# Kernel optimization log

Hardware: AMD Instinct MI355X
Metric: run time of the kernel (lower is better)

Reference implementation:

```python
import jax, jax.numpy as jnp
import numpy as np
import math

B, T, D = 8, 1024, 1024
N, L = 256, 768
H = 16
TE = 2048  # time_embed_dim
EPS = 1e-5


def _ln(x, g, b):
    mu = jnp.mean(x, axis=-1, keepdims=True)
    var = jnp.mean(jnp.square(x - mu), axis=-1, keepdims=True)
    return (x - mu) * jax.lax.rsqrt(var + EPS) * g + b


def setup_inputs() -> dict:
    key = jax.random.key(0)
    ks = jax.random.split(key, 16)
    s = lambda fan_in: 1.0 / math.sqrt(fan_in)
    return {
        "x": jax.random.normal(ks[0], (B, T, D), jnp.float32),
        "xf": jax.random.normal(ks[1], (B, N, L), jnp.float32),
        "emb": jax.random.normal(ks[2], (B, TE), jnp.float32),
        "ln_g": jnp.ones((D,), jnp.float32),
        "ln_b": jnp.zeros((D,), jnp.float32),
        "cln_g": jnp.ones((L,), jnp.float32),
        "cln_b": jnp.zeros((L,), jnp.float32),
        "Wq": jax.random.normal(ks[3], (D, D), jnp.float32) * s(D),
        "bq": jnp.zeros((D,), jnp.float32),
        "Wk": jax.random.normal(ks[4], (L, D), jnp.float32) * s(L),
        "bk": jnp.zeros((D,), jnp.float32),
        "Wv": jax.random.normal(ks[5], (L, D), jnp.float32) * s(L),
        "bv": jnp.zeros((D,), jnp.float32),
        "sln_g": jnp.ones((D,), jnp.float32),
        "sln_b": jnp.zeros((D,), jnp.float32),
        "Wemb": jax.random.normal(ks[6], (TE, 2 * D), jnp.float32) * s(TE),
        "bemb": jnp.zeros((2 * D,), jnp.float32),
        "Wout": jax.random.normal(ks[7], (D, D), jnp.float32) * s(D) * 0.02,
        "bout": jnp.zeros((D,), jnp.float32),
    }


def reference(x, xf, emb, ln_g, ln_b, cln_g, cln_b, Wq, bq, Wk, bk, Wv, bv,
              sln_g, sln_b, Wemb, bemb, Wout, bout):
    # x: (B,T,D), xf: (B,N,L), emb: (B,TE)
    hd = D // H
    q = (_ln(x, ln_g, ln_b) @ Wq + bq).reshape(B, T, H, hd)
    xf_n = _ln(xf, cln_g, cln_b)
    k = (xf_n @ Wk + bk).reshape(B, N, H, hd)
    v = (xf_n @ Wv + bv).reshape(B, N, H, hd)
    # scores: (B,T,N,H); note: scaled by sqrt(D//H)
    att = jnp.einsum('bthd,bnhd->btnh', q, k) / math.sqrt(hd)
    w = jax.nn.softmax(att, axis=2)  # softmax over conditioning tokens N
    y = jnp.einsum('btnh,bnhd->bthd', w, v).reshape(B, T, D)
    # StylizationBlock (dropout = 0)
    emb_out = jax.nn.silu(emb) @ Wemb + bemb  # (B, 2D)
    scale, shift = jnp.split(emb_out[:, None, :], 2, axis=2)
    h = _ln(y, sln_g, sln_b) * (1.0 + scale) + shift
    h = jax.nn.silu(h) @ Wout + bout
    return x + h
```

## Files before the change

### kernel.cpp

```cpp
#include <hip/hip_runtime.h>
#include <hip/hip_bf16.h>

typedef __hip_bfloat16 bf16;
typedef unsigned short ushort;
typedef unsigned char uchar;
typedef long i64;
typedef __attribute__((ext_vector_type(4))) float f32x4;

#define B_ 8
#define T_ 1024
#define D_ 1024
#define N_ 256
#define L_ 768
#define H_ 16
#define HD_ 64
#define TE_ 2048

__device__ __forceinline__ void gld16(const void* g, void* l) {
    __builtin_amdgcn_global_load_lds((const __attribute__((address_space(1))) void*)g,
                                     (__attribute__((address_space(3))) void*)l,
                                     16, 0, 0);
}

__device__ __forceinline__ float bitf(unsigned u) { return __uint_as_float(u); }

__device__ __forceinline__ int pk4_fp8(float a, float b, float c, float d) {
    int p = __builtin_amdgcn_cvt_pk_fp8_f32(a, b, 0, false);
    p = __builtin_amdgcn_cvt_pk_fp8_f32(c, d, p, true);
    return p;
}
__device__ __forceinline__ uchar pk1_fp8(float a) {
    int p = __builtin_amdgcn_cvt_pk_fp8_f32(a, a, 0, false);
    return (uchar)(p & 0xff);
}
__device__ __forceinline__ float dec8(uchar b) {
    int e = (b >> 3) & 15, m = b & 7;
    float mag = e ? (float)(8 + m) * bitf((unsigned)(117 + e) << 23)
                  : (float)m * bitf(118u << 23);
    return (b & 0x80) ? -mag : mag;
}

template <int NV>
__device__ __forceinline__ void ln_row(const float* __restrict__ rp,
                                       const float* __restrict__ g,
                                       const float* __restrict__ bb,
                                       uchar* __restrict__ op, int lane) {
    float4 va[NV];
#pragma unroll
    for (int i = 0; i < NV; i++) va[i] = ((const float4*)rp)[i * 64 + lane];
    float s = 0.f, s2 = 0.f;
#pragma unroll
    for (int i = 0; i < NV; i++) {
        s  += va[i].x + va[i].y + va[i].z + va[i].w;
        s2 += va[i].x * va[i].x + va[i].y * va[i].y + va[i].z * va[i].z + va[i].w * va[i].w;
    }
#pragma unroll
    for (int off = 32; off; off >>= 1) {
        s  += __shfl_xor(s,  off, 64);
        s2 += __shfl_xor(s2, off, 64);
    }
    const float inv_n = 1.f / (float)(NV * 256);
    float mu = s * inv_n;
    float var = s2 * inv_n - mu * mu;
    float rstd = rsqrtf(var + 1e-5f);
#pragma unroll
    for (int i = 0; i < NV; i++) {
        float4 gv = ((const float4*)g)[i * 64 + lane];
        float4 bv = ((const float4*)bb)[i * 64 + lane];
        ((int*)op)[i * 64 + lane] = pk4_fp8((va[i].x - mu) * rstd * gv.x + bv.x,
                                            (va[i].y - mu) * rstd * gv.y + bv.y,
                                            (va[i].z - mu) * rstd * gv.z + bv.z,
                                            (va[i].w - mu) * rstd * gv.w + bv.w);
    }
}

__global__ __launch_bounds__(256) void prep_kernel(
        const float* __restrict__ x, const float* __restrict__ xf,
        const float* __restrict__ g1, const float* __restrict__ b1,
        const float* __restrict__ g2, const float* __restrict__ b2,
        const float* __restrict__ Wq, const float* __restrict__ Wk,
        const float* __restrict__ Wv, const float* __restrict__ Wo,
        const float* __restrict__ emb, const float* __restrict__ Wemb,
        uchar* __restrict__ xn8, uchar* __restrict__ xfn8,
        uchar* __restrict__ wq8, uchar* __restrict__ wk8,
        uchar* __restrict__ wv8, uchar* __restrict__ wo8,
        float* __restrict__ part) {
    __shared__ __align__(16) char smem[16384];
    int bid = blockIdx.x;
    int tid = threadIdx.x;
    if (bid < 2560) {
        int w = tid >> 6, lane = tid & 63;
        int row = bid * 4 + w;
        if (row < B_ * T_) {
            ln_row<4>(x + (size_t)row * D_, g1, b1, xn8 + (size_t)row * D_, lane);
        } else {
            int r = row - B_ * T_;
            ln_row<3>(xf + (size_t)r * L_, g2, b2, xfn8 + (size_t)r * L_, lane);
        }
    } else if (bid < 3456) {
        uchar (*t)[65] = (uchar(*)[65])smem;
        int id = bid - 2560;
        int xb = id & 15, y = id >> 4;
        const float* W; uchar* Wt; int K, ky;
        if (y < 16)      { W = Wq; Wt = wq8; K = 1024; ky = y; }
        else if (y < 28) { W = Wk; Wt = wk8; K = 768;  ky = y - 16; }
        else if (y < 40) { W = Wv; Wt = wv8; K = 768;  ky = y - 28; }
        else             { W = Wo; Wt = wo8; K = 1024; ky = y - 40; }
        int k0 = ky * 64, n0 = xb * 64;
#pragma unroll
        for (int i = 0; i < 16; i++) {
            int e = tid + i * 256;
            int r = e >> 6, c = e & 63;
            t[r][c] = pk1_fp8(W[(size_t)(k0 + r) * D_ + n0 + c]);
        }
        __syncthreads();
#pragma unroll
        for (int i = 0; i < 4; i++) {
            int e = tid + i * 256;
            int r = e >> 4, cg = (e & 15) * 4;
            unsigned u = (unsigned)t[cg][r] | ((unsigned)t[cg + 1][r] << 8)
                       | ((unsigned)t[cg + 2][r] << 16) | ((unsigned)t[cg + 3][r] << 24);
            *(unsigned*)&Wt[(size_t)(n0 + r) * K + k0 + cg] = u;
        }
    } else {
        float* se  = (float*)smem;
        float* red = (float*)(smem + 8192);
        int id = bid - 3456;
        int j0 = (id & 31) * 64;
        int ks = id >> 5;
        int tx = tid & 15, ty = tid >> 4;
        int w = tid >> 6, lane = tid & 63;
#pragma unroll
        for (int b = 0; b < 8; b++) {
            float xv = emb[b * TE_ + ks * 256 + tid];
            se[b * 256 + tid] = xv / (1.f + __expf(-xv));
        }
        __syncthreads();
        float acc[8][4] = {};
#pragma unroll 4
        for (int i = 0; i < 16; i++) {
            int e = ty + 16 * i;
            float4 wv = *(const float4*)&Wemb[(size_t)(ks * 256 + e) * 2048 + j0 + tx * 4];
#pragma unroll
            for (int b = 0; b < 8; b++) {
                float s = se[b * 256 + e];
                acc[b][0] += s * wv.x; acc[b][1] += s * wv.y;
                acc[b][2] += s * wv.z; acc[b][3] += s * wv.w;
            }
        }
#pragma unroll
        for (int b = 0; b < 8; b++)
#pragma unroll
            for (int m = 0; m < 4; m++) {
                float v = acc[b][m];
                v += __shfl_down(v, 32, 64);
                v += __shfl_down(v, 16, 64);
                if (lane < 16) red[(w * 8 + b) * 64 + lane * 4 + m] = v;
            }
        __syncthreads();
        for (int o = tid; o < 512; o += 256) {
            int b = o >> 6, jl = o & 63;
            float s = red[(0 * 8 + b) * 64 + jl] + red[(1 * 8 + b) * 64 + jl]
                    + red[(2 * 8 + b) * 64 + jl] + red[(3 * 8 + b) * 64 + jl];
            part[((size_t)ks * 8 + b) * 2048 + j0 + jl] = s;
        }
    }
}

template <int MODE>
__device__ __forceinline__ void gemm_body(const uchar* __restrict__ Ap,
                                          const uchar* __restrict__ Bp,
                                          const float* __restrict__ bias,
                                          const float* __restrict__ res,
                                          void* __restrict__ Cout,
                                          int m0, int n0, int Ncols, int K,
                                          uchar* SH) {
    int tid = threadIdx.x;
    int w = tid >> 6, lane = tid & 63;
    int quad = lane >> 4, l15 = lane & 15;
    int wm = (w >> 1) * 64, wn = (w & 1) * 64;
    int lr4 = lane >> 2;
    int sp4 = lane & 3;
    uchar* A0 = SH;
    uchar* B0 = SH + 8192;
    uchar* A1 = SH + 16384;
    uchar* B1 = SH + 24576;
    f32x4 acc[4][4] = {};

    auto stage = [&](int kt, uchar* As, uchar* Bs) {
#pragma unroll
        for (int j = 0; j < 2; j++) {
            int r = w * 32 + j * 16 + lr4;
            int gc = sp4 ^ (r & 3);
            gld16(&Ap[(size_t)(m0 + r) * K + kt + gc * 16], &As[(w * 32 + j * 16) * 64]);
        }
#pragma unroll
        for (int j = 0; j < 2; j++) {
            int r = w * 32 + j * 16 + lr4;
            int gc = sp4 ^ (r & 3);
            gld16(&Bp[(size_t)(n0 + r) * K + kt + gc * 16], &Bs[(w * 32 + j * 16) * 64]);
        }
    };
    auto compute = [&](const uchar* As, const uchar* Bs) {
#pragma unroll
        for (int kh = 0; kh < 2; kh++) {
            int c4 = kh * 2 + (quad >> 1);
            int sub = (quad & 1) * 8;
            int pos = (c4 ^ (l15 & 3)) * 16 + sub;
            i64 af[4], bfr[4];
#pragma unroll
            for (int mt = 0; mt < 4; mt++)
                af[mt] = *(const i64*)&As[(wm + mt * 16 + l15) * 64 + pos];
#pragma unroll
            for (int nt = 0; nt < 4; nt++)
                bfr[nt] = *(const i64*)&Bs[(wn + nt * 16 + l15) * 64 + pos];
#pragma unroll
            for (int mt = 0; mt < 4; mt++)
#pragma unroll
                for (int nt = 0; nt < 4; nt++)
                    acc[mt][nt] = __builtin_amdgcn_mfma_f32_16x16x32_fp8_fp8(af[mt], bfr[nt], acc[mt][nt], 0, 0, 0);
        }
    };

    int nt2 = K >> 6;
    stage(0, A0, B0);
    __syncthreads();
    for (int t = 0; t + 2 <= nt2; t += 2) {
        stage((t + 1) * 64, A1, B1);
        compute(A0, B0);
        __syncthreads();
        if (t + 2 < nt2) stage((t + 2) * 64, A0, B0);
        compute(A1, B1);
        __syncthreads();
    }

    if (MODE == 0) {
#pragma unroll
        for (int mt = 0; mt < 4; mt++)
#pragma unroll
            for (int nt = 0; nt < 4; nt++)
#pragma unroll
                for (int reg = 0; reg < 4; reg++) {
                    int rl = wm + mt * 16 + quad * 4 + reg;
                    int cl = wn + nt * 16 + l15;
                    SH[rl * 128 + cl] = pk1_fp8(acc[mt][nt][reg] + bias[n0 + cl]);
                }
        __syncthreads();
#pragma unroll
        for (int i = 0; i < 4; i++) {
            int row = (tid >> 3) + i * 32;
            int ch = (tid & 7) * 16;
            *(int4*)&((uchar*)Cout)[(size_t)(m0 + row) * Ncols + n0 + ch] =
                *(const int4*)&SH[row * 128 + ch];
        }
    } else {
#pragma unroll
        for (int mt = 0; mt < 4; mt++) {
#pragma unroll
            for (int nt = 0; nt < 4; nt++) {
#pragma unroll
                for (int reg = 0; reg < 4; reg++) {
                    int row = m0 + wm + mt * 16 + quad * 4 + reg;
                    int col = n0 + wn + nt * 16 + l15;
                    float v = acc[mt][nt][reg] + bias[col];
                    if (MODE == 1) {
                        v += res[(size_t)row * Ncols + col];
                        ((float*)Cout)[(size_t)row * Ncols + col] = v;
                    } else {
                        int b = row >> 8, n = row & 255;
                        int h = col >> 6, d = col & 63;
                        size_t addr = ((size_t)(b * 16 + h)) * 16384 + (size_t)d * 256
                                    + (((n >> 4) ^ (d & 15)) * 16) + (n & 15);
                        ((uchar*)Cout)[addr] = pk1_fp8(v);
                    }
                }
            }
        }
    }
}

__global__ __launch_bounds__(256, 4) void qkv_gemm(const uchar* __restrict__ xn8,
                                                   const uchar* __restrict__ xfn8,
                                                   const uchar* __restrict__ wq8,
                                                   const uchar* __restrict__ wk8,
                                                   const uchar* __restrict__ wv8,
                                                   const float* __restrict__ bq,
                                                   const float* __restrict__ bk,
                                                   const float* __restrict__ bv,
                                                   uchar* __restrict__ q8,
                                                   uchar* __restrict__ k8,
                                                   uchar* __restrict__ vT8,
                                                   const float* __restrict__ part,
                                                   const float* __restrict__ bemb,
                                                   float* __restrict__ embo) {
    __shared__ __align__(16) uchar SH[32768];
    int bid = blockIdx.x;
    if (bid < 512) {
        gemm_body<0>(xn8, wq8, bq, nullptr, q8,
                     (bid & 63) * 128, (bid >> 6) * 128, D_, D_, SH);
    } else if (bid < 640) {
        int id = bid - 512;
        gemm_body<0>(xfn8, wk8, bk, nullptr, k8,
                     (id & 15) * 128, (id >> 4) * 128, D_, L_, SH);
    } else if (bid < 768) {
        int id = bid - 640;
        gemm_body<2>(xfn8, wv8, bv, nullptr, vT8,
                     (id & 15) * 128, (id >> 4) * 128, D_, L_, SH);
    } else {
        int o = (bid - 768) * 256 + threadIdx.x;
        int b = o >> 11, j = o & 2047;
        float s = bemb[j];
#pragma unroll
        for (int ks = 0; ks < 8; ks++) s += part[((size_t)ks * 8 + b) * 2048 + j];
        embo[o] = s;
    }
}

__global__ __launch_bounds__(256, 4) void out_gemm(const uchar* __restrict__ a8,
                                                   const uchar* __restrict__ wo8,
                                                   const float* __restrict__ bout,
                                                   const float* __restrict__ x,
                                                   float* __restrict__ out) {
    __shared__ __align__(16) uchar SH[32768];
    int bid = blockIdx.x;
    gemm_body<1>(a8, wo8, bout, x, out,
                 (bid & 63) * 128, (bid >> 6) * 128, D_, D_, SH);
}

__global__ __launch_bounds__(256) void attn_mfma(const uchar* __restrict__ q8,
                                                 const uchar* __restrict__ k8,
                                                 const uchar* __restrict__ vT8,
                                                 uchar* __restrict__ y8) {
    __shared__ __align__(16) uchar KV[16384];
    __shared__ __align__(16) uchar P[16384];
    int tid = threadIdx.x;
    int w = tid >> 6, lane = tid & 63;
    int quad = lane >> 4, l15 = lane & 15;
    int bid = blockIdx.x;
    int work = (bid & 7) * 256 + (bid >> 3);
    int t0 = (work & 15) * 64;
    int bh = work >> 4;
    int b = bh >> 4, h = bh & 15;
    int lln = lane >> 3, sp = lane & 7;

#pragma unroll
    for (int j = 0; j < 4; j++) {
        int dn = w * 32 + j * 8 + lln;
        int c8 = sp ^ (dn & 7);
        int n = dn * 2 + (c8 >> 2);
        gld16(&k8[(size_t)(b * N_ + n) * D_ + h * 64 + (c8 & 3) * 16],
              &KV[(w * 32 + j * 8) * 128]);
    }
#pragma unroll
    for (int j = 0; j < 2; j++) {
        int r = w * 16 + j * 8 + lln;
        int c = (sp ^ (r & 7)) & 3;
        gld16(&q8[(size_t)(b * T_ + t0 + r) * D_ + h * 64 + c * 16],
              &P[(w * 16 + j * 8) * 128]);
    }
    __syncthreads();

    int qrow = w * 16 + l15;
    i64 aq[2];
#pragma unroll
    for (int kk2 = 0; kk2 < 2; kk2++) {
        int chunk = kk2 * 2 + (quad >> 1);
        aq[kk2] = *(const i64*)&P[qrow * 128 + ((chunk ^ (qrow & 7)) * 16) + (quad & 1) * 8];
    }
    f32x4 sf[16];
#pragma unroll
    for (int nt = 0; nt < 16; nt++) {
        int n = nt * 16 + l15;
        int dn = n >> 1, hn = n & 1;
        int c80 = (hn * 4 + 0 + (quad >> 1)) ^ (dn & 7);
        int c81 = (hn * 4 + 2 + (quad >> 1)) ^ (dn & 7);
        i64 b0 = *(const i64*)&KV[dn * 128 + c80 * 16 + (quad & 1) * 8];
        i64 b1 = *(const i64*)&KV[dn * 128 + c81 * 16 + (quad & 1) * 8];
        f32x4 z = {};
        f32x4 t = __builtin_amdgcn_mfma_f32_16x16x32_fp8_fp8(aq[0], b0, z, 0, 0, 0);
        sf[nt] = __builtin_amdgcn_mfma_f32_16x16x32_fp8_fp8(aq[1], b1, t, 0, 0, 0);
    }
    __syncthreads();

    const uchar* vbase = vT8 + (size_t)(b * 16 + h) * 16384;
#pragma unroll
    for (int j = 0; j < 4; j++) {
        gld16(&vbase[(w * 4 + j) * 1024 + lane * 16], &KV[(w * 4 + j) * 1024]);
    }

    const float scale = 0.125f;
    float sm[4] = {0.f, 0.f, 0.f, 0.f};
#pragma unroll
    for (int nt = 0; nt < 16; nt++)
#pragma unroll
        for (int reg = 0; reg < 4; reg++) {
            float e = __expf(sf[nt][reg] * scale);
            sf[nt][reg] = e;
            sm[reg] += e;
        }
#pragma unroll
    for (int off = 1; off < 16; off <<= 1)
#pragma unroll
        for (int reg = 0; reg < 4; reg++)
            sm[reg] += __shfl_xor(sm[reg], off, 64);
    float inv[4];
#pragma unroll
    for (int reg = 0; reg < 4; reg++) inv[reg] = 1.f / sm[reg];

#pragma unroll
    for (int nt = 0; nt < 16; nt++)
#pragma unroll
        for (int reg = 0; reg < 4; reg++) {
            int r = w * 16 + quad * 4 + reg;
            int n = nt * 16 + l15;
            P[r * 256 + (((n >> 4) ^ (r & 15)) * 16) + (n & 15)] = pk1_fp8(sf[nt][reg]);
        }
    __syncthreads();

    f32x4 of[4] = {};
    int prow = w * 16 + l15;
#pragma unroll
    for (int kk = 0; kk < 8; kk++) {
        int ck = kk * 2 + (quad >> 1);
        i64 ap = *(const i64*)&P[prow * 256 + ((ck ^ (prow & 15)) * 16) + (quad & 1) * 8];
#pragma unroll
        for (int dt = 0; dt < 4; dt++) {
            int d = dt * 16 + l15;
            i64 bv = *(const i64*)&KV[d * 256 + ((ck ^ (d & 15)) * 16) + (quad & 1) * 8];
            of[dt] = __builtin_amdgcn_mfma_f32_16x16x32_fp8_fp8(ap, bv, of[dt], 0, 0, 0);
        }
    }
    __syncthreads();
#pragma unroll
    for (int dt = 0; dt < 4; dt++)
#pragma unroll
        for (int reg = 0; reg < 4; reg++) {
            int rl = w * 16 + quad * 4 + reg;
            P[rl * 64 + dt * 16 + l15] = pk1_fp8(of[dt][reg] * inv[reg]);
        }
    __syncthreads();
    {
        int row = tid >> 2, ch = (tid & 3) * 16;
        *(int4*)&y8[(size_t)(b * T_ + t0 + row) * D_ + h * 64 + ch] =
            *(const int4*)&P[row * 64 + ch];
    }
}

__global__ __launch_bounds__(256) void styl_kernel(const uchar* __restrict__ y8,
                                                   const float* __restrict__ g,
                                                   const float* __restrict__ bb,
                                                   const float* __restrict__ embo,
                                                   uchar* __restrict__ a8) {
    int tid = threadIdx.x, w = tid >> 6, lane = tid & 63;
    int row = blockIdx.x * 4 + w;
    int b = row >> 10;
    const uchar* rp = y8 + (size_t)row * D_;
    uchar* op = a8 + (size_t)row * D_;
    float v[16];
    float s = 0.f, s2 = 0.f;
#pragma unroll
    for (int i = 0; i < 4; i++) {
        unsigned u = ((const unsigned*)rp)[i * 64 + lane];
#pragma unroll
        for (int j = 0; j < 4; j++) {
            float f = dec8((uchar)(u >> (8 * j)));
            v[i * 4 + j] = f; s += f; s2 += f * f;
        }
    }
#pragma unroll
    for (int off = 32; off; off >>= 1) {
        s  += __shfl_xor(s,  off, 64);
        s2 += __shfl_xor(s2, off, 64);
    }
    float mu = s * (1.f / 1024.f);
    float rstd = rsqrtf(s2 * (1.f / 1024.f) - mu * mu + 1e-5f);
#pragma unroll
    for (int i = 0; i < 4; i++) {
        int c4 = i * 64 + lane;
        float4 gv  = ((const float4*)g)[c4];
        float4 bv  = ((const float4*)bb)[c4];
        float4 scv = ((const float4*)(embo + b * 2048))[c4];
        float4 shv = ((const float4*)(embo + b * 2048 + 1024))[c4];
        float h0 = (v[i*4+0] - mu) * rstd * gv.x + bv.x;
        float h1 = (v[i*4+1] - mu) * rstd * gv.y + bv.y;
        float h2 = (v[i*4+2] - mu) * rstd * gv.z + bv.z;
        float h3 = (v[i*4+3] - mu) * rstd * gv.w + bv.w;
        h0 = h0 * (1.f + scv.x) + shv.x;
        h1 = h1 * (1.f + scv.y) + shv.y;
        h2 = h2 * (1.f + scv.z) + shv.z;
        h3 = h3 * (1.f + scv.w) + shv.w;
        h0 = h0 / (1.f + __expf(-h0));
        h1 = h1 / (1.f + __expf(-h1));
        h2 = h2 / (1.f + __expf(-h2));
        h3 = h3 / (1.f + __expf(-h3));
        ((int*)op)[c4] = pk4_fp8(h0, h1, h2, h3);
    }
}

extern "C" void kernel_launch(void* const* d_in, const int* in_sizes, int n_in,
                              void* d_out, int out_size, void* d_ws, size_t ws_size,
                              hipStream_t stream) {
    const float* x    = (const float*)d_in[0];
    const float* xf   = (const float*)d_in[1];
    const float* emb  = (const float*)d_in[2];
    const float* ln_g = (const float*)d_in[3];
    const float* ln_b = (const float*)d_in[4];
    const float* cln_g= (const float*)d_in[5];
    const float* cln_b= (const float*)d_in[6];
    const float* Wq   = (const float*)d_in[7];
    const float* bq   = (const float*)d_in[8];
    const float* Wk   = (const float*)d_in[9];
    const float* bk   = (const float*)d_in[10];
    const float* Wv   = (const float*)d_in[11];
    const float* bv   = (const float*)d_in[12];
    const float* sln_g= (const float*)d_in[13];
    const float* sln_b= (const float*)d_in[14];
    const float* Wemb = (const float*)d_in[15];
    const float* bemb = (const float*)d_in[16];
    const float* Wout = (const float*)d_in[17];
    const float* bout = (const float*)d_in[18];
    float* out = (float*)d_out;

    char* wsp = (char*)d_ws;
    const size_t MB = 1024 * 1024;
    uchar* xn8  = (uchar*)(wsp);
    uchar* xfn8 = (uchar*)(wsp + 8 * MB);
    uchar* wq8  = (uchar*)(wsp + 10 * MB);
    uchar* wk8  = (uchar*)(wsp + 11 * MB);
    uchar* wv8  = (uchar*)(wsp + 12 * MB);
    uchar* wo8  = (uchar*)(wsp + 13 * MB);
    uchar* q8   = (uchar*)(wsp + 14 * MB);
    uchar* k8   = (uchar*)(wsp + 22 * MB);
    uchar* vT8  = (uchar*)(wsp + 24 * MB);
    uchar* y8   = (uchar*)(wsp + 26 * MB);
    uchar* a8   = (uchar*)(wsp + 34 * MB);
    float* embo = (float*)(wsp + 42 * MB);
    float* part = (float*)(wsp + 43 * MB);

    prep_kernel<<<3712, 256, 0, stream>>>(x, xf, ln_g, ln_b, cln_g, cln_b,
                                          Wq, Wk, Wv, Wout, emb, Wemb,
                                          xn8, xfn8, wq8, wk8, wv8, wo8, part);

    qkv_gemm<<<832, 256, 0, stream>>>(xn8, xfn8, wq8, wk8, wv8, bq, bk, bv,
                                      q8, k8, vT8, part, bemb, embo);

    attn_mfma<<<2048, 256, 0, stream>>>(q8, k8, vT8, y8);

    styl_kernel<<<2048, 256, 0, stream>>>(y8, sln_g, sln_b, embo, a8);

    out_gemm<<<512, 256, 0, stream>>>(a8, wo8, bout, x, out);
}
```

Before: 233.8 us.

## Transpose attention MFMA operands to keep softmax probabilities in registers

Swaps the A/B operands of the QK^T MFMA so each lane holds a query's scores across keys, which turns the row-sum into two cross-lane shuffles. The exponentiated probabilities are packed to fp8 and redistributed with lane shuffles straight into MFMA operand registers for the PV product, removing the LDS round trip for P and one barrier. The output tile is written to LDS with an XOR swizzle, and the P buffer shrinks to 8 KB, lowering LDS use. The cost is extra shuffle and select instructions inside the PV loop.

```diff
diff --git a/kernel.cpp b/kernel.cpp
--- a/kernel.cpp
+++ b/kernel.cpp
@@ -332,7 +332,7 @@
                                                  const uchar* __restrict__ vT8,
                                                  uchar* __restrict__ y8) {
     __shared__ __align__(16) uchar KV[16384];
-    __shared__ __align__(16) uchar P[16384];
+    __shared__ __align__(16) uchar P[8192];
     int tid = threadIdx.x;
     int w = tid >> 6, lane = tid & 63;
     int quad = lane >> 4, l15 = lane & 15;
@@ -361,12 +361,14 @@
     __syncthreads();
 
     int qrow = w * 16 + l15;
-    i64 aq[2];
-#pragma unroll
-    for (int kk2 = 0; kk2 < 2; kk2++) {
-        int chunk = kk2 * 2 + (quad >> 1);
-        aq[kk2] = *(const i64*)&P[qrow * 128 + ((chunk ^ (qrow & 7)) * 16) + (quad & 1) * 8];
-    }
+    i64 aq0, aq1;
+    {
+        int c0 = (quad >> 1);
+        int c1 = 2 + (quad >> 1);
+        aq0 = *(const i64*)&P[qrow * 128 + ((c0 ^ (qrow & 7)) * 16) + (quad & 1) * 8];
+        aq1 = *(const i64*)&P[qrow * 128 + ((c1 ^ (qrow & 7)) * 16) + (quad & 1) * 8];
+    }
+
     f32x4 sf[16];
 #pragma unroll
     for (int nt = 0; nt < 16; nt++) {
@@ -377,8 +379,8 @@
         i64 b0 = *(const i64*)&KV[dn * 128 + c80 * 16 + (quad & 1) * 8];
         i64 b1 = *(const i64*)&KV[dn * 128 + c81 * 16 + (quad & 1) * 8];
         f32x4 z = {};
-        f32x4 t = __builtin_amdgcn_mfma_f32_16x16x32_fp8_fp8(aq[0], b0, z, 0, 0, 0);
-        sf[nt] = __builtin_amdgcn_mfma_f32_16x16x32_fp8_fp8(aq[1], b1, t, 0, 0, 0);
+        f32x4 t = __builtin_amdgcn_mfma_f32_16x16x32_fp8_fp8(b0, aq0, z, 0, 0, 0);
+        sf[nt] = __builtin_amdgcn_mfma_f32_16x16x32_fp8_fp8(b1, aq1, t, 0, 0, 0);
     }
     __syncthreads();
 
@@ -389,60 +391,52 @@
     }
 
     const float scale = 0.125f;
-    float sm[4] = {0.f, 0.f, 0.f, 0.f};
+    float sm = 0.f;
 #pragma unroll
     for (int nt = 0; nt < 16; nt++)
 #pragma unroll
         for (int reg = 0; reg < 4; reg++) {
             float e = __expf(sf[nt][reg] * scale);
             sf[nt][reg] = e;
-            sm[reg] += e;
-        }
-#pragma unroll
-    for (int off = 1; off < 16; off <<= 1)
-#pragma unroll
-        for (int reg = 0; reg < 4; reg++)
-            sm[reg] += __shfl_xor(sm[reg], off, 64);
-    float inv[4];
-#pragma unroll
-    for (int reg = 0; reg < 4; reg++) inv[reg] = 1.f / sm[reg];
-
-#pragma unroll
-    for (int nt = 0; nt < 16; nt++)
-#pragma unroll
-        for (int reg = 0; reg < 4; reg++) {
-            int r = w * 16 + quad * 4 + reg;
-            int n = nt * 16 + l15;
-            P[r * 256 + (((n >> 4) ^ (r & 15)) * 16) + (n & 15)] = pk1_fp8(sf[nt][reg]);
-        }
+            sm += e;
+        }
+    sm += __shfl_xor(sm, 16, 64);
+    sm += __shfl_xor(sm, 32, 64);
+    float inv = 1.f / sm;
     __syncthreads();
 
     f32x4 of[4] = {};
-    int prow = w * 16 + l15;
+    int srcLo = 32 * (quad & 1) + l15;
 #pragma unroll
     for (int kk = 0; kk < 8; kk++) {
+        int pkA = pk4_fp8(sf[2 * kk][0], sf[2 * kk][1], sf[2 * kk][2], sf[2 * kk][3]);
+        int pkB = pk4_fp8(sf[2 * kk + 1][0], sf[2 * kk + 1][1], sf[2 * kk + 1][2], sf[2 * kk + 1][3]);
+        int loA = __shfl(pkA, srcLo, 64);
+        int hiA = __shfl(pkA, srcLo + 16, 64);
+        int loB = __shfl(pkB, srcLo, 64);
+        int hiB = __shfl(pkB, srcLo + 16, 64);
+        unsigned lo = (quad >> 1) ? (unsigned)loB : (unsigned)loA;
+        unsigned hi = (quad >> 1) ? (unsigned)hiB : (unsigned)hiA;
+        i64 pf = (i64)(((unsigned long long)hi << 32) | (unsigned long long)lo);
         int ck = kk * 2 + (quad >> 1);
-        i64 ap = *(const i64*)&P[prow * 256 + ((ck ^ (prow & 15)) * 16) + (quad & 1) * 8];
 #pragma unroll
         for (int dt = 0; dt < 4; dt++) {
             int d = dt * 16 + l15;
             i64 bv = *(const i64*)&KV[d * 256 + ((ck ^ (d & 15)) * 16) + (quad & 1) * 8];
-            of[dt] = __builtin_amdgcn_mfma_f32_16x16x32_fp8_fp8(ap, bv, of[dt], 0, 0, 0);
-        }
-    }
-    __syncthreads();
-#pragma unroll
-    for (int dt = 0; dt < 4; dt++)
-#pragma unroll
-        for (int reg = 0; reg < 4; reg++) {
-            int rl = w * 16 + quad * 4 + reg;
-            P[rl * 64 + dt * 16 + l15] = pk1_fp8(of[dt][reg] * inv[reg]);
-        }
+            of[dt] = __builtin_amdgcn_mfma_f32_16x16x32_fp8_fp8(bv, pf, of[dt], 0, 0, 0);
+        }
+    }
+
+#pragma unroll
+    for (int dt = 0; dt < 4; dt++) {
+        int ov = pk4_fp8(of[dt][0] * inv, of[dt][1] * inv, of[dt][2] * inv, of[dt][3] * inv);
+        *(int*)&P[qrow * 64 + ((dt ^ (l15 & 3)) * 16) + quad * 4] = ov;
+    }
     __syncthreads();
     {
-        int row = tid >> 2, ch = (tid & 3) * 16;
-        *(int4*)&y8[(size_t)(b * T_ + t0 + row) * D_ + h * 64 + ch] =
-            *(const int4*)&P[row * 64 + ch];
+        int row = tid >> 2, c = tid & 3;
+        *(int4*)&y8[(size_t)(b * T_ + t0 + row) * D_ + h * 64 + c * 16] =
+            *(const int4*)&P[row * 64 + ((c ^ (row & 3)) * 16)];
     }
 }
 
```

After: 229.7 us (median of 2 runs). Within noise of the previous version (-1.8%).
